# Kernel tuning notes

Measured on AMD Instinct MI355X. Metric: run time of the kernel, lower is better.

## Reference

```python
import jax, jax.numpy as jnp
import numpy as np

B, LQ, LV = 32, 64, 128
QS, FS, BN = 512, 1024, 512

def setup_inputs() -> dict:
    key = jax.random.key(0)
    k1, k2, k3, k4, k5 = jax.random.split(key, 5)
    s = lambda n: 1.0 / np.sqrt(n)
    return {
        "phr_feats": jax.random.normal(k1, (B, LQ, QS), dtype=jnp.float32),
        "vis_feats": jax.random.normal(k2, (B, LV, FS), dtype=jnp.float32),
        "W": jax.random.uniform(k3, (BN, QS), jnp.float32, -s(QS), s(QS)),
        "U": jax.random.uniform(k4, (BN, FS), jnp.float32, -s(FS), s(FS)),
        "b": jnp.ones((BN,), dtype=jnp.float32),
        "w": jax.random.uniform(k5, (1, BN), jnp.float32, -s(BN), s(BN)),
    }

def reference(phr_feats, vis_feats, W, U, b, w):
    # Wh: [B,Lq,BN], Uv: [B,Lv,BN]
    Wh = jnp.einsum('bqd,nd->bqn', phr_feats, W)
    Uv = jnp.einsum('bvf,nf->bvn', vis_feats, U)
    # broadcast add + tanh: [B,Lq,Lv,BN]
    t = jnp.tanh(Wh[:, :, None, :] + Uv[:, None, :, :] + b)
    energies = jnp.einsum('bqvn,n->bqv', t, w[0])  # squeeze(-1)
    weights = jax.nn.softmax(energies, axis=2)
    aligned = jnp.einsum('bqv,bvf->bqf', weights, vis_feats)
    semantic_group_feats = jnp.concatenate([phr_feats, aligned], axis=2)
    return (semantic_group_feats, weights, energies)
```

## Files before the change

### kernel.cpp

```cpp
#include <hip/hip_runtime.h>

#define NB  32
#define NLQ 64
#define NLV 128
#define NQS 512
#define NFS 1024
#define NBN 512
#define CC  2.8853900817779268f

typedef float  floatx4 __attribute__((ext_vector_type(4)));
typedef __bf16 bf16x8  __attribute__((ext_vector_type(8)));
typedef unsigned short us;

__device__ __forceinline__ us f2bf(float f) {
    unsigned int u = __float_as_uint(f);
    u += 0x7fffu + ((u >> 16) & 1u);
    return (us)(u >> 16);
}
__device__ __forceinline__ unsigned int pktrunc(float lo, float hi) {
    return __builtin_amdgcn_perm(__float_as_uint(hi), __float_as_uint(lo), 0x07060302u);
}
__device__ __forceinline__ float blo(unsigned int u) {
    return __uint_as_float(u << 16);
}
__device__ __forceinline__ float bhi(unsigned int u) {
    return __uint_as_float(u & 0xffff0000u);
}

#define PHR4 262144
#define VIS4 1048576
#define WW4  65536
#define UU4  131072
#define TOT4 (PHR4 + VIS4 + WW4 + UU4)

__global__ __launch_bounds__(256) void convert_bf16(
    const float* __restrict__ phr, const float* __restrict__ vis,
    const float* __restrict__ W,   const float* __restrict__ U,
    us* __restrict__ phr_b, us* __restrict__ vis_b,
    us* __restrict__ W_b,   us* __restrict__ U_b,
    float* __restrict__ out_sgf)
{
    int i = blockIdx.x * 256 + threadIdx.x;
    if (i >= TOT4) return;
    const float* src; us* dst; int o;
    if (i < PHR4)              { src = phr; dst = phr_b; o = i; }
    else if (i < PHR4 + VIS4)  { src = vis; dst = vis_b; o = i - PHR4; }
    else if (i < PHR4 + VIS4 + WW4) { src = W; dst = W_b; o = i - PHR4 - VIS4; }
    else                       { src = U; dst = U_b; o = i - PHR4 - VIS4 - WW4; }
    float4 v = ((const float4*)src)[o];
    uint2 r = { pktrunc(v.x, v.y), pktrunc(v.z, v.w) };
    *(uint2*)(dst + (size_t)o * 4) = r;
    if (i < PHR4) {
        int row = o >> 7, c4 = o & 127;
        ((float4*)out_sgf)[(size_t)row * 384 + c4] = v;
    }
}

__device__ __forceinline__ void gemm64(
    us* As, us* Bs,
    const us* __restrict__ A, const us* __restrict__ Bt,
    const float* __restrict__ bias, us* __restrict__ C,
    int K, int bx, int by, int hasb)
{
    const int tid  = threadIdx.x;
    const int m0   = bx * 64;
    const int n0   = by * 64;
    const int wave = tid >> 6;
    const int lane = tid & 63;
    const int wm   = (wave >> 1) * 32;
    const int wn   = (wave & 1) * 32;
    const int srow = tid >> 2;
    const int sk   = (tid & 3) * 8;
    const int fm   = lane & 15;
    const int fko  = (lane >> 4) * 8;

    floatx4 acc[2][2] = {};
    const us* ag = A  + (size_t)(m0 + srow) * K + sk;
    const us* bg = Bt + (size_t)(n0 + srow) * K + sk;

    uint4 av = *(const uint4*)(ag);
    uint4 bv = *(const uint4*)(bg);

    for (int k0 = 0; k0 < K; k0 += 32) {
        __syncthreads();
        *(uint4*)(As + srow * 40 + sk) = av;
        *(uint4*)(Bs + srow * 40 + sk) = bv;
        const int kn = k0 + 32;
        if (kn < K) {
            av = *(const uint4*)(ag + kn);
            bv = *(const uint4*)(bg + kn);
        }
        __syncthreads();
        bf16x8 am[2], bn[2];
        #pragma unroll
        for (int i = 0; i < 2; ++i)
            am[i] = *(const bf16x8*)(As + (wm + 16 * i + fm) * 40 + fko);
        #pragma unroll
        for (int j = 0; j < 2; ++j)
            bn[j] = *(const bf16x8*)(Bs + (wn + 16 * j + fm) * 40 + fko);
        #pragma unroll
        for (int i = 0; i < 2; ++i)
            #pragma unroll
            for (int j = 0; j < 2; ++j)
                acc[i][j] = __builtin_amdgcn_mfma_f32_16x16x32_bf16(am[i], bn[j], acc[i][j], 0, 0, 0);
    }

    const int cr = (lane >> 4) * 4;
    const int cc = lane & 15;
    #pragma unroll
    for (int i = 0; i < 2; ++i)
        #pragma unroll
        for (int j = 0; j < 2; ++j)
            #pragma unroll
            for (int r = 0; r < 4; ++r) {
                int gm = m0 + wm + 16 * i + cr + r;
                int gn = n0 + wn + 16 * j + cc;
                float v = acc[i][j][r];
                if (hasb) v += bias[gn];
                C[(size_t)gm * NBN + gn] = f2bf(__builtin_amdgcn_exp2f(CC * v));
            }
}

__global__ __launch_bounds__(256) void gemm_both(
    const us* __restrict__ phr_b, const us* __restrict__ W_b,
    const float* __restrict__ bias,
    const us* __restrict__ vis_b, const us* __restrict__ U_b,
    us* __restrict__ whY, us* __restrict__ uvY)
{
    __shared__ __align__(16) us As[64 * 40];
    __shared__ __align__(16) us Bs[64 * 40];
    int blk = blockIdx.x;
    if (blk < 256) {
        gemm64(As, Bs, phr_b, W_b, bias, whY, NQS, blk % 32, blk / 32, 1);
    } else {
        blk -= 256;
        gemm64(As, Bs, vis_b, U_b, bias, uvY, NFS, blk % 64, blk / 64, 0);
    }
}

__global__ __launch_bounds__(256) void energize(
    const us* __restrict__ whY,
    const us* __restrict__ uvY,
    const float* __restrict__ wvec,
    float* __restrict__ p_ws, float* __restrict__ out_w, float* __restrict__ out_e)
{
    const float LOG2E = 1.4426950408889634f;
    const int blk  = blockIdx.x;
    const int q    = blk >> 5;
    const int b    = blk & 31;
    const int row  = b * NLQ + q;
    const int tid  = threadIdx.x;
    const int wave = tid >> 6;
    const int lane = tid & 63;

    __shared__ float e_s[128];

    const int n0 = lane << 3;
    uint4 yq4 = *(const uint4*)(whY + (size_t)row * NBN + n0);
    float Yq[8] = { blo(yq4.x), bhi(yq4.x), blo(yq4.y), bhi(yq4.y),
                    blo(yq4.z), bhi(yq4.z), blo(yq4.w), bhi(yq4.w) };
    float4 w0 = *(const float4*)(wvec + n0);
    float4 w1 = *(const float4*)(wvec + n0 + 4);
    float nw2[8] = { 2.f*w0.x, 2.f*w0.y, 2.f*w0.z, 2.f*w0.w,
                     2.f*w1.x, 2.f*w1.y, 2.f*w1.z, 2.f*w1.w };
    float sumw = w0.x + w0.y + w0.z + w0.w + w1.x + w1.y + w1.z + w1.w;
    #pragma unroll
    for (int off = 32; off; off >>= 1) sumw += __shfl_xor(sumw, off);

    #pragma unroll
    for (int vblk = 0; vblk < 4; ++vblk) {
        const us* base = uvY + ((size_t)b * NLV + wave * 32 + vblk * 8) * NBN + n0;
        float s[8];
        #pragma unroll
        for (int j = 0; j < 8; ++j) {
            uint4 u = *(const uint4*)(base + (size_t)j * NBN);
            float acc = 0.f;
            auto term = [&](unsigned int uu, int k) {
                float d0 = fmaf(blo(uu), Yq[k],     1.f);
                float d1 = fmaf(bhi(uu), Yq[k + 1], 1.f);
                acc = fmaf(nw2[k],     __builtin_amdgcn_rcpf(d0), acc);
                acc = fmaf(nw2[k + 1], __builtin_amdgcn_rcpf(d1), acc);
            };
            term(u.x, 0); term(u.y, 2); term(u.z, 4); term(u.w, 6);
            s[j] = acc;
        }
        #pragma unroll
        for (int m = 8; m <= 32; m <<= 1)
            #pragma unroll
            for (int j = 0; j < 8; ++j) s[j] += __shfl_xor(s[j], m);
        float t[4];
        #pragma unroll
        for (int p = 0; p < 4; ++p) {
            float ae = s[2*p]     + __shfl_xor(s[2*p],     1);
            float bo = s[2*p + 1] + __shfl_xor(s[2*p + 1], 1);
            t[p] = (lane & 1) ? bo : ae;
        }
        float u2[2];
        #pragma unroll
        for (int p = 0; p < 2; ++p) {
            float ae = t[2*p]     + __shfl_xor(t[2*p],     2);
            float bo = t[2*p + 1] + __shfl_xor(t[2*p + 1], 2);
            u2[p] = (lane & 2) ? bo : ae;
        }
        {
            float ae = u2[0] + __shfl_xor(u2[0], 4);
            float bo = u2[1] + __shfl_xor(u2[1], 4);
            float r  = (lane & 4) ? bo : ae;
            if (lane < 8) e_s[wave * 32 + vblk * 8 + lane] = sumw - r;
        }
    }
    __syncthreads();

    if (wave == 0) {
        float e0 = e_s[lane];
        float e1 = e_s[lane + 64];
        float m = fmaxf(e0, e1);
        #pragma unroll
        for (int off = 32; off; off >>= 1) m = fmaxf(m, __shfl_xor(m, off));
        float x0 = __builtin_amdgcn_exp2f((e0 - m) * LOG2E);
        float x1 = __builtin_amdgcn_exp2f((e1 - m) * LOG2E);
        float ss = x0 + x1;
        #pragma unroll
        for (int off = 32; off; off >>= 1) ss += __shfl_xor(ss, off);
        float inv = __builtin_amdgcn_rcpf(ss);
        float p0 = x0 * inv, p1 = x1 * inv;
        size_t o = (size_t)row * NLV;
        p_ws[o + lane]       = p0;
        p_ws[o + lane + 64]  = p1;
        out_w[o + lane]      = p0;
        out_w[o + lane + 64] = p1;
        out_e[o + lane]      = e0;
        out_e[o + lane + 64] = e1;
    }
}

__global__ __launch_bounds__(256) void aligned_k(
    const us* __restrict__ vis_b,
    const float* __restrict__ p_ws,
    float* __restrict__ out_sgf)
{
    const int blk = blockIdx.x;
    const int b   = blk & 31;
    const int qg  = blk >> 5;
    const int tid = threadIdx.x;

    __shared__ float p_s[4][128];
    if (tid < 128) {
        const float* src = p_ws + (size_t)(b * NLQ + qg * 4) * NLV;
        ((float4*)&p_s[0][0])[tid] = ((const float4*)src)[tid];
    }
    __syncthreads();

    const int f0 = tid * 4;
    float4 acc[4] = {};
    const us* vb = vis_b + (size_t)b * NLV * NFS + f0;
    for (int v0 = 0; v0 < NLV; v0 += 4) {
        float4 pv[4];
        #pragma unroll
        for (int qq = 0; qq < 4; ++qq) pv[qq] = *(const float4*)&p_s[qq][v0];
        #pragma unroll
        for (int dv = 0; dv < 4; ++dv) {
            uint2 u = *(const uint2*)(vb + (size_t)(v0 + dv) * NFS);
            float x0 = blo(u.x), x1 = bhi(u.x), x2 = blo(u.y), x3 = bhi(u.y);
            #pragma unroll
            for (int qq = 0; qq < 4; ++qq) {
                float p = (dv == 0) ? pv[qq].x : (dv == 1) ? pv[qq].y
                        : (dv == 2) ? pv[qq].z : pv[qq].w;
                acc[qq].x = fmaf(p, x0, acc[qq].x);
                acc[qq].y = fmaf(p, x1, acc[qq].y);
                acc[qq].z = fmaf(p, x2, acc[qq].z);
                acc[qq].w = fmaf(p, x3, acc[qq].w);
            }
        }
    }
    #pragma unroll
    for (int qq = 0; qq < 4; ++qq) {
        size_t row = (size_t)(b * NLQ + qg * 4 + qq);
        *(float4*)(out_sgf + row * (NQS + NFS) + NQS + f0) = acc[qq];
    }
}

extern "C" void kernel_launch(void* const* d_in, const int* in_sizes, int n_in,
                              void* d_out, int out_size, void* d_ws, size_t ws_size,
                              hipStream_t stream) {
    const float* phr  = (const float*)d_in[0];
    const float* vis  = (const float*)d_in[1];
    const float* W    = (const float*)d_in[2];
    const float* U    = (const float*)d_in[3];
    const float* bias = (const float*)d_in[4];
    const float* wvec = (const float*)d_in[5];

    char* ws = (char*)d_ws;
    us* phr_b = (us*)ws;
    us* vis_b = (us*)(ws + (2u << 20));
    us* W_b   = (us*)(ws + (10u << 20));
    us* U_b   = (us*)(ws + (10u << 20) + (512u << 10));
    us* whY   = (us*)(ws + (12u << 20));
    us* uvY   = (us*)(ws + (14u << 20));
    float* p_ws = (float*)(ws + (18u << 20));

    float* out     = (float*)d_out;
    float* out_sgf = out;
    float* out_w   = out_sgf + (size_t)NB * NLQ * (NQS + NFS);
    float* out_e   = out_w   + (size_t)NB * NLQ * NLV;

    convert_bf16<<<(TOT4 + 255) / 256, 256, 0, stream>>>(
        phr, vis, W, U, phr_b, vis_b, W_b, U_b, out_sgf);
    gemm_both<<<768, 256, 0, stream>>>(phr_b, W_b, bias, vis_b, U_b, whY, uvY);
    energize<<<NB * NLQ, 256, 0, stream>>>(whY, uvY, wvec, p_ws, out_w, out_e);
    aligned_k<<<NB * 16, 256, 0, stream>>>(vis_b, p_ws, out_sgf);
}
```

Measured before the change: 132.8 us.

## Fuse bf16 conversion into GEMM and merge energy/softmax/aligned kernels

Removes the separate fp32-to-bf16 conversion kernel: the GEMM now loads fp32 inputs and packs them to bf16 in registers before staging into LDS. The energy, softmax and aligned-sum kernels are merged into one 512-thread kernel. Each block handles 4 query rows, so every uvY load is reused across 4 queries, and the softmax weights pass through LDS instead of a global workspace. The aligned product and the phrase copy now read fp32 vis/phr directly. This cuts launches and intermediate global traffic, at the cost of doubling GEMM input load bytes and more register pressure in the fused kernel.

Result: faster. 128.8 us (-3.0%).

```diff
diff --git a/kernel.cpp b/kernel.cpp
--- a/kernel.cpp
+++ b/kernel.cpp
@@ -27,38 +27,9 @@
     return __uint_as_float(u & 0xffff0000u);
 }
 
-#define PHR4 262144
-#define VIS4 1048576
-#define WW4  65536
-#define UU4  131072
-#define TOT4 (PHR4 + VIS4 + WW4 + UU4)
-
-__global__ __launch_bounds__(256) void convert_bf16(
-    const float* __restrict__ phr, const float* __restrict__ vis,
-    const float* __restrict__ W,   const float* __restrict__ U,
-    us* __restrict__ phr_b, us* __restrict__ vis_b,
-    us* __restrict__ W_b,   us* __restrict__ U_b,
-    float* __restrict__ out_sgf)
-{
-    int i = blockIdx.x * 256 + threadIdx.x;
-    if (i >= TOT4) return;
-    const float* src; us* dst; int o;
-    if (i < PHR4)              { src = phr; dst = phr_b; o = i; }
-    else if (i < PHR4 + VIS4)  { src = vis; dst = vis_b; o = i - PHR4; }
-    else if (i < PHR4 + VIS4 + WW4) { src = W; dst = W_b; o = i - PHR4 - VIS4; }
-    else                       { src = U; dst = U_b; o = i - PHR4 - VIS4 - WW4; }
-    float4 v = ((const float4*)src)[o];
-    uint2 r = { pktrunc(v.x, v.y), pktrunc(v.z, v.w) };
-    *(uint2*)(dst + (size_t)o * 4) = r;
-    if (i < PHR4) {
-        int row = o >> 7, c4 = o & 127;
-        ((float4*)out_sgf)[(size_t)row * 384 + c4] = v;
-    }
-}
-
 __device__ __forceinline__ void gemm64(
     us* As, us* Bs,
-    const us* __restrict__ A, const us* __restrict__ Bt,
+    const float* __restrict__ A, const float* __restrict__ Bt,
     const float* __restrict__ bias, us* __restrict__ C,
     int K, int bx, int by, int hasb)
 {
@@ -75,20 +46,24 @@
     const int fko  = (lane >> 4) * 8;
 
     floatx4 acc[2][2] = {};
-    const us* ag = A  + (size_t)(m0 + srow) * K + sk;
-    const us* bg = Bt + (size_t)(n0 + srow) * K + sk;
-
-    uint4 av = *(const uint4*)(ag);
-    uint4 bv = *(const uint4*)(bg);
+    const float* ag = A  + (size_t)(m0 + srow) * K + sk;
+    const float* bg = Bt + (size_t)(n0 + srow) * K + sk;
+
+    float4 a0 = *(const float4*)(ag),     a1 = *(const float4*)(ag + 4);
+    float4 b0 = *(const float4*)(bg),     b1 = *(const float4*)(bg + 4);
 
     for (int k0 = 0; k0 < K; k0 += 32) {
         __syncthreads();
+        uint4 av = { pktrunc(a0.x, a0.y), pktrunc(a0.z, a0.w),
+                     pktrunc(a1.x, a1.y), pktrunc(a1.z, a1.w) };
+        uint4 bv = { pktrunc(b0.x, b0.y), pktrunc(b0.z, b0.w),
+                     pktrunc(b1.x, b1.y), pktrunc(b1.z, b1.w) };
         *(uint4*)(As + srow * 40 + sk) = av;
         *(uint4*)(Bs + srow * 40 + sk) = bv;
         const int kn = k0 + 32;
         if (kn < K) {
-            av = *(const uint4*)(ag + kn);
-            bv = *(const uint4*)(bg + kn);
+            a0 = *(const float4*)(ag + kn); a1 = *(const float4*)(ag + kn + 4);
+            b0 = *(const float4*)(bg + kn); b1 = *(const float4*)(bg + kn + 4);
         }
         __syncthreads();
         bf16x8 am[2], bn[2];
@@ -122,43 +97,51 @@
 }
 
 __global__ __launch_bounds__(256) void gemm_both(
-    const us* __restrict__ phr_b, const us* __restrict__ W_b,
+    const float* __restrict__ phr, const float* __restrict__ W,
     const float* __restrict__ bias,
-    const us* __restrict__ vis_b, const us* __restrict__ U_b,
+    const float* __restrict__ vis, const float* __restrict__ U,
     us* __restrict__ whY, us* __restrict__ uvY)
 {
     __shared__ __align__(16) us As[64 * 40];
     __shared__ __align__(16) us Bs[64 * 40];
     int blk = blockIdx.x;
     if (blk < 256) {
-        gemm64(As, Bs, phr_b, W_b, bias, whY, NQS, blk % 32, blk / 32, 1);
+        gemm64(As, Bs, phr, W, bias, whY, NQS, blk % 32, blk / 32, 1);
     } else {
         blk -= 256;
-        gemm64(As, Bs, vis_b, U_b, bias, uvY, NFS, blk % 64, blk / 64, 0);
-    }
-}
-
-__global__ __launch_bounds__(256) void energize(
+        gemm64(As, Bs, vis, U, bias, uvY, NFS, blk % 64, blk / 64, 0);
+    }
+}
+
+__global__ __launch_bounds__(512, 4) void attn_fused(
     const us* __restrict__ whY,
     const us* __restrict__ uvY,
     const float* __restrict__ wvec,
-    float* __restrict__ p_ws, float* __restrict__ out_w, float* __restrict__ out_e)
+    const float* __restrict__ phr,
+    const float* __restrict__ vis,
+    float* __restrict__ out_sgf, float* __restrict__ out_w, float* __restrict__ out_e)
 {
     const float LOG2E = 1.4426950408889634f;
     const int blk  = blockIdx.x;
-    const int q    = blk >> 5;
     const int b    = blk & 31;
-    const int row  = b * NLQ + q;
+    const int qg   = blk >> 5;
     const int tid  = threadIdx.x;
     const int wave = tid >> 6;
     const int lane = tid & 63;
 
-    __shared__ float e_s[128];
+    __shared__ float e_s[4][128];
+    __shared__ float p_s[4][128];
 
     const int n0 = lane << 3;
-    uint4 yq4 = *(const uint4*)(whY + (size_t)row * NBN + n0);
-    float Yq[8] = { blo(yq4.x), bhi(yq4.x), blo(yq4.y), bhi(yq4.y),
-                    blo(yq4.z), bhi(yq4.z), blo(yq4.w), bhi(yq4.w) };
+    float Yq[4][8];
+    #pragma unroll
+    for (int qq = 0; qq < 4; ++qq) {
+        uint4 y = *(const uint4*)(whY + (size_t)(b * NLQ + qg * 4 + qq) * NBN + n0);
+        Yq[qq][0] = blo(y.x); Yq[qq][1] = bhi(y.x);
+        Yq[qq][2] = blo(y.y); Yq[qq][3] = bhi(y.y);
+        Yq[qq][4] = blo(y.z); Yq[qq][5] = bhi(y.z);
+        Yq[qq][6] = blo(y.w); Yq[qq][7] = bhi(y.w);
+    }
     float4 w0 = *(const float4*)(wvec + n0);
     float4 w1 = *(const float4*)(wvec + n0 + 4);
     float nw2[8] = { 2.f*w0.x, 2.f*w0.y, 2.f*w0.z, 2.f*w0.w,
@@ -168,52 +151,57 @@
     for (int off = 32; off; off >>= 1) sumw += __shfl_xor(sumw, off);
 
     #pragma unroll
-    for (int vblk = 0; vblk < 4; ++vblk) {
-        const us* base = uvY + ((size_t)b * NLV + wave * 32 + vblk * 8) * NBN + n0;
-        float s[8];
+    for (int vblk = 0; vblk < 2; ++vblk) {
+        const us* base = uvY + ((size_t)b * NLV + wave * 16 + vblk * 8) * NBN + n0;
+        float s[4][8];
         #pragma unroll
         for (int j = 0; j < 8; ++j) {
             uint4 u = *(const uint4*)(base + (size_t)j * NBN);
-            float acc = 0.f;
-            auto term = [&](unsigned int uu, int k) {
-                float d0 = fmaf(blo(uu), Yq[k],     1.f);
-                float d1 = fmaf(bhi(uu), Yq[k + 1], 1.f);
-                acc = fmaf(nw2[k],     __builtin_amdgcn_rcpf(d0), acc);
-                acc = fmaf(nw2[k + 1], __builtin_amdgcn_rcpf(d1), acc);
-            };
-            term(u.x, 0); term(u.y, 2); term(u.z, 4); term(u.w, 6);
-            s[j] = acc;
-        }
-        #pragma unroll
-        for (int m = 8; m <= 32; m <<= 1)
-            #pragma unroll
-            for (int j = 0; j < 8; ++j) s[j] += __shfl_xor(s[j], m);
-        float t[4];
-        #pragma unroll
-        for (int p = 0; p < 4; ++p) {
-            float ae = s[2*p]     + __shfl_xor(s[2*p],     1);
-            float bo = s[2*p + 1] + __shfl_xor(s[2*p + 1], 1);
-            t[p] = (lane & 1) ? bo : ae;
-        }
-        float u2[2];
-        #pragma unroll
-        for (int p = 0; p < 2; ++p) {
-            float ae = t[2*p]     + __shfl_xor(t[2*p],     2);
-            float bo = t[2*p + 1] + __shfl_xor(t[2*p + 1], 2);
-            u2[p] = (lane & 2) ? bo : ae;
-        }
-        {
+            float yv[8] = { blo(u.x), bhi(u.x), blo(u.y), bhi(u.y),
+                            blo(u.z), bhi(u.z), blo(u.w), bhi(u.w) };
+            #pragma unroll
+            for (int qq = 0; qq < 4; ++qq) {
+                float a = 0.f;
+                #pragma unroll
+                for (int k = 0; k < 8; ++k) {
+                    float d = fmaf(yv[k], Yq[qq][k], 1.f);
+                    a = fmaf(nw2[k], __builtin_amdgcn_rcpf(d), a);
+                }
+                s[qq][j] = a;
+            }
+        }
+        #pragma unroll
+        for (int qq = 0; qq < 4; ++qq) {
+            #pragma unroll
+            for (int m = 8; m <= 32; m <<= 1)
+                #pragma unroll
+                for (int j = 0; j < 8; ++j) s[qq][j] += __shfl_xor(s[qq][j], m);
+            float t[4];
+            #pragma unroll
+            for (int p = 0; p < 4; ++p) {
+                float ae = s[qq][2*p]     + __shfl_xor(s[qq][2*p],     1);
+                float bo = s[qq][2*p + 1] + __shfl_xor(s[qq][2*p + 1], 1);
+                t[p] = (lane & 1) ? bo : ae;
+            }
+            float u2[2];
+            #pragma unroll
+            for (int p = 0; p < 2; ++p) {
+                float ae = t[2*p]     + __shfl_xor(t[2*p],     2);
+                float bo = t[2*p + 1] + __shfl_xor(t[2*p + 1], 2);
+                u2[p] = (lane & 2) ? bo : ae;
+            }
             float ae = u2[0] + __shfl_xor(u2[0], 4);
             float bo = u2[1] + __shfl_xor(u2[1], 4);
             float r  = (lane & 4) ? bo : ae;
-            if (lane < 8) e_s[wave * 32 + vblk * 8 + lane] = sumw - r;
+            if (lane < 8) e_s[qq][wave * 16 + vblk * 8 + lane] = sumw - r;
         }
     }
     __syncthreads();
 
-    if (wave == 0) {
-        float e0 = e_s[lane];
-        float e1 = e_s[lane + 64];
+    if (wave < 4) {
+        const int q = wave;
+        float e0 = e_s[q][lane];
+        float e1 = e_s[q][lane + 64];
         float m = fmaxf(e0, e1);
         #pragma unroll
         for (int off = 32; off; off >>= 1) m = fmaxf(m, __shfl_xor(m, off));
@@ -224,59 +212,46 @@
         for (int off = 32; off; off >>= 1) ss += __shfl_xor(ss, off);
         float inv = __builtin_amdgcn_rcpf(ss);
         float p0 = x0 * inv, p1 = x1 * inv;
-        size_t o = (size_t)row * NLV;
-        p_ws[o + lane]       = p0;
-        p_ws[o + lane + 64]  = p1;
+        size_t o = (size_t)(b * NLQ + qg * 4 + q) * NLV;
         out_w[o + lane]      = p0;
         out_w[o + lane + 64] = p1;
         out_e[o + lane]      = e0;
         out_e[o + lane + 64] = e1;
-    }
-}
-
-__global__ __launch_bounds__(256) void aligned_k(
-    const us* __restrict__ vis_b,
-    const float* __restrict__ p_ws,
-    float* __restrict__ out_sgf)
-{
-    const int blk = blockIdx.x;
-    const int b   = blk & 31;
-    const int qg  = blk >> 5;
-    const int tid = threadIdx.x;
-
-    __shared__ float p_s[4][128];
-    if (tid < 128) {
-        const float* src = p_ws + (size_t)(b * NLQ + qg * 4) * NLV;
-        ((float4*)&p_s[0][0])[tid] = ((const float4*)src)[tid];
+        p_s[q][lane]      = p0;
+        p_s[q][lane + 64] = p1;
+    } else {
+        const int qq = wave - 4;
+        const size_t r = (size_t)(b * NLQ + qg * 4 + qq);
+        const float4* src = (const float4*)(phr + r * NQS);
+        float4* dst = (float4*)(out_sgf + r * (NQS + NFS));
+        dst[lane]      = src[lane];
+        dst[lane + 64] = src[lane + 64];
     }
     __syncthreads();
 
-    const int f0 = tid * 4;
-    float4 acc[4] = {};
-    const us* vb = vis_b + (size_t)b * NLV * NFS + f0;
+    const int f0 = tid << 1;
+    float2 acc[4] = {};
+    const float* vb = vis + (size_t)b * NLV * NFS + f0;
     for (int v0 = 0; v0 < NLV; v0 += 4) {
         float4 pv[4];
         #pragma unroll
         for (int qq = 0; qq < 4; ++qq) pv[qq] = *(const float4*)&p_s[qq][v0];
         #pragma unroll
         for (int dv = 0; dv < 4; ++dv) {
-            uint2 u = *(const uint2*)(vb + (size_t)(v0 + dv) * NFS);
-            float x0 = blo(u.x), x1 = bhi(u.x), x2 = blo(u.y), x3 = bhi(u.y);
+            float2 x = *(const float2*)(vb + (size_t)(v0 + dv) * NFS);
             #pragma unroll
             for (int qq = 0; qq < 4; ++qq) {
                 float p = (dv == 0) ? pv[qq].x : (dv == 1) ? pv[qq].y
                         : (dv == 2) ? pv[qq].z : pv[qq].w;
-                acc[qq].x = fmaf(p, x0, acc[qq].x);
-                acc[qq].y = fmaf(p, x1, acc[qq].y);
-                acc[qq].z = fmaf(p, x2, acc[qq].z);
-                acc[qq].w = fmaf(p, x3, acc[qq].w);
+                acc[qq].x = fmaf(p, x.x, acc[qq].x);
+                acc[qq].y = fmaf(p, x.y, acc[qq].y);
             }
         }
     }
     #pragma unroll
     for (int qq = 0; qq < 4; ++qq) {
         size_t row = (size_t)(b * NLQ + qg * 4 + qq);
-        *(float4*)(out_sgf + row * (NQS + NFS) + NQS + f0) = acc[qq];
+        *(float2*)(out_sgf + row * (NQS + NFS) + NQS + f0) = acc[qq];
     }
 }
 
@@ -291,22 +266,15 @@
     const float* wvec = (const float*)d_in[5];
 
     char* ws = (char*)d_ws;
-    us* phr_b = (us*)ws;
-    us* vis_b = (us*)(ws + (2u << 20));
-    us* W_b   = (us*)(ws + (10u << 20));
-    us* U_b   = (us*)(ws + (10u << 20) + (512u << 10));
-    us* whY   = (us*)(ws + (12u << 20));
-    us* uvY   = (us*)(ws + (14u << 20));
-    float* p_ws = (float*)(ws + (18u << 20));
+    us* whY = (us*)ws;
+    us* uvY = (us*)(ws + (2u << 20));
 
     float* out     = (float*)d_out;
     float* out_sgf = out;
     float* out_w   = out_sgf + (size_t)NB * NLQ * (NQS + NFS);
     float* out_e   = out_w   + (size_t)NB * NLQ * NLV;
 
-    convert_bf16<<<(TOT4 + 255) / 256, 256, 0, stream>>>(
-        phr, vis, W, U, phr_b, vis_b, W_b, U_b, out_sgf);
-    gemm_both<<<768, 256, 0, stream>>>(phr_b, W_b, bias, vis_b, U_b, whY, uvY);
-    energize<<<NB * NLQ, 256, 0, stream>>>(whY, uvY, wvec, p_ws, out_w, out_e);
-    aligned_k<<<NB * 16, 256, 0, stream>>>(vis_b, p_ws, out_sgf);
-}
+    gemm_both<<<768, 256, 0, stream>>>(phr, W, bias, vis, U, whY, uvY);
+    attn_fused<<<NB * 16, 512, 0, stream>>>(whY, uvY, wvec, phr, vis,
+                                            out_sgf, out_w, out_e);
+}
```
